# Optimization experiments

Measured on AMD Instinct MI355X. Metric: run time of the kernel, lower is better.

## Reference

```python
import math
import jax, jax.numpy as jnp
import numpy as np

B, H, HKV, L, S, D = 1, 32, 8, 2048, 2048, 128
N_REP = H // HKV          # 4
SCALE = 1.0 / math.sqrt(D)


def setup_inputs() -> dict:
    key = jax.random.key(0)
    k1, k2, k3, k4 = jax.random.split(key, 4)
    query = jax.random.normal(k1, (B, H, L, D), dtype=jnp.float32)
    k_ = jax.random.normal(k2, (B, HKV, S, D), dtype=jnp.float32)
    v_ = jax.random.normal(k3, (B, HKV, S, D), dtype=jnp.float32)
    attn_mask = jax.random.normal(k4, (B, 1, L, S), dtype=jnp.float32)
    return {"query": query, "key": k_, "value": v_, "attn_mask": attn_mask}


def reference(query, key, value, attn_mask):
    # repeat_kv: Q -> [B, HKV, n_rep, L, D]; K/V stay [B, HKV, S, D]
    # (the torch code reshapes K/V to [B, HKV, 1, S, D]; broadcasting via
    # einsum is equivalent), mask unsqueezed at dim 1 -> [B, 1, 1, L, S].
    q = query.reshape(B, HKV, N_REP, L, D)
    scores = jnp.einsum("bkrld,bksd->bkrls", q, key)          # [B,HKV,n_rep,L,S]
    scores = scores + attn_mask[:, None]                        # broadcast add
    # softmax_fp8(x, dim=-1, invAttnHead=1/sqrt(D)) scales input by invAttnHead
    w = jax.nn.softmax(scores * SCALE, axis=-1)
    # dropout_p = 0.0 -> identity
    out = jnp.einsum("bkrls,bksd->bkrld", w, value)             # [B,HKV,n_rep,L,D]
    return out
```

## Files before the change

### kernel.cpp

```cpp
#include <hip/hip_runtime.h>

#define NH   32
#define NKV  8
#define LQ   2048
#define SK   2048
#define DH   128
#define BM   128
#define BN   64
#define KSTRIDE 136
#define VSTRIDE 72
#define PSTRIDE 72

typedef __attribute__((ext_vector_type(8)))  short bf8;
typedef __attribute__((ext_vector_type(4)))  float f4;
typedef __attribute__((ext_vector_type(16))) float f16v;

#if __has_builtin(__builtin_amdgcn_exp2f)
#define EXP2F(x) __builtin_amdgcn_exp2f(x)
#else
#define EXP2F(x) exp2f(x)
#endif

__device__ __forceinline__ unsigned short f2bf(float f) {
    unsigned int u = __builtin_bit_cast(unsigned int, f);
    u = (u + 0x7FFFu + ((u >> 16) & 1u)) >> 16;
    return (unsigned short)u;
}

__global__ __launch_bounds__(256) void convert_k_kernel(
    const float* __restrict__ K, unsigned short* __restrict__ Kb)
{
    size_t base = ((size_t)blockIdx.x * 256 + threadIdx.x) * 8;
    float4 a = *(const float4*)(K + base);
    float4 b = *(const float4*)(K + base + 4);
    bf8 o;
    o[0] = (short)f2bf(a.x); o[1] = (short)f2bf(a.y);
    o[2] = (short)f2bf(a.z); o[3] = (short)f2bf(a.w);
    o[4] = (short)f2bf(b.x); o[5] = (short)f2bf(b.y);
    o[6] = (short)f2bf(b.z); o[7] = (short)f2bf(b.w);
    *(bf8*)(Kb + base) = o;
}

__global__ __launch_bounds__(256) void transpose_v_kernel(
    const float* __restrict__ V, unsigned short* __restrict__ VTb)
{
    __shared__ __align__(16) unsigned short Vl[DH * VSTRIDE];
    const int tid = threadIdx.x;
    const int kv  = blockIdx.x >> 5;
    const int s0  = (blockIdx.x & 31) * 64;
    const float* Vh = V + (size_t)kv * SK * DH;

    #pragma unroll
    for (int i = 0; i < 8; ++i) {
        int idx = tid * 4 + i * 1024;
        int s = idx >> 7, d = idx & 127;
        const float4 v4 = *(const float4*)(Vh + (size_t)(s0 + s) * DH + d);
        Vl[(d + 0) * VSTRIDE + s] = f2bf(v4.x);
        Vl[(d + 1) * VSTRIDE + s] = f2bf(v4.y);
        Vl[(d + 2) * VSTRIDE + s] = f2bf(v4.z);
        Vl[(d + 3) * VSTRIDE + s] = f2bf(v4.w);
    }
    __syncthreads();
    unsigned short* out = VTb + (size_t)kv * DH * SK;
    #pragma unroll
    for (int i = 0; i < 4; ++i) {
        int c = tid + i * 256;
        int d = c >> 3, s8 = (c & 7) * 8;
        *(bf8*)(out + (size_t)d * SK + s0 + s8) = *(const bf8*)(Vl + d * VSTRIDE + s8);
    }
}

__global__ __launch_bounds__(256, 2) void fattn_kernel(
    const float* __restrict__ Q, const unsigned short* __restrict__ Kb,
    const unsigned short* __restrict__ VTb, const float* __restrict__ M,
    float* __restrict__ O)
{
    __shared__ __align__(16) unsigned short Klds[BN * KSTRIDE];
    __shared__ __align__(16) unsigned short Vlds[DH * VSTRIDE];
    __shared__ __align__(16) unsigned short Plds[4 * 32 * PSTRIDE];

    const int tid  = threadIdx.x;
    const int wave = tid >> 6;
    const int lane = tid & 63;
    const int l32  = lane & 31;
    const int hh   = lane >> 5;

    const int bx = blockIdx.x;
    const int h  = bx >> 4;
    const int lt = bx & 15;
    const int q0 = lt * BM;
    const int kv = h >> 2;

    const float*          Qh  = Q   + (size_t)h  * LQ * DH;
    const unsigned short* Kh  = Kb  + (size_t)kv * SK * DH;
    const unsigned short* VTh = VTb + (size_t)kv * DH * SK;

    const int qrow = q0 + wave * 32 + l32;
    const float* Mq = M + (size_t)qrow * SK;

    bf8 bQ[8];
    #pragma unroll
    for (int ks = 0; ks < 8; ++ks) {
        const float* qp = Qh + (size_t)qrow * DH + ks * 16 + hh * 8;
        float4 a = *(const float4*)(qp);
        float4 b = *(const float4*)(qp + 4);
        bQ[ks][0] = (short)f2bf(a.x); bQ[ks][1] = (short)f2bf(a.y);
        bQ[ks][2] = (short)f2bf(a.z); bQ[ks][3] = (short)f2bf(a.w);
        bQ[ks][4] = (short)f2bf(b.x); bQ[ks][5] = (short)f2bf(b.y);
        bQ[ks][6] = (short)f2bf(b.z); bQ[ks][7] = (short)f2bf(b.w);
    }

    f16v accO[4];
    #pragma unroll
    for (int nt = 0; nt < 4; ++nt)
        #pragma unroll
        for (int r = 0; r < 16; ++r) accO[nt][r] = 0.f;
    float lpart = 0.f;

    const float scale_log2e = 0.08838834764831845f * 1.4426950408889634f;

    unsigned short* Pw = Plds + wave * 32 * PSTRIDE;

    for (int s0 = 0; s0 < SK; s0 += BN) {
        __syncthreads();
        #pragma unroll
        for (int c = 0; c < 4; ++c) {
            int chunk = tid + c * 256;
            int sK = chunk >> 4, dK = (chunk & 15) * 8;
            *(bf8*)(Klds + sK * KSTRIDE + dK) =
                *(const bf8*)(Kh + (size_t)(s0 + sK) * DH + dK);
            int dV = chunk >> 3, sV = (chunk & 7) * 8;
            *(bf8*)(Vlds + dV * VSTRIDE + sV) =
                *(const bf8*)(VTh + (size_t)dV * SK + s0 + sV);
        }
        float4 mv[2][4];
        #pragma unroll
        for (int mt = 0; mt < 2; ++mt)
            #pragma unroll
            for (int grp = 0; grp < 4; ++grp)
                mv[mt][grp] = *(const float4*)(Mq + s0 + mt * 32 + grp * 8 + hh * 4);
        __syncthreads();

        f16v accS[2];
        #pragma unroll
        for (int mt = 0; mt < 2; ++mt) {
            f16v a;
            #pragma unroll
            for (int r = 0; r < 16; ++r) a[r] = 0.f;
            #pragma unroll
            for (int ks = 0; ks < 8; ++ks) {
                bf8 aK = *(const bf8*)(Klds + (mt * 32 + l32) * KSTRIDE + ks * 16 + hh * 8);
                a = __builtin_amdgcn_mfma_f32_32x32x16_bf16(aK, bQ[ks], a, 0, 0, 0);
            }
            accS[mt] = a;
        }

        #pragma unroll
        for (int mt = 0; mt < 2; ++mt) {
            #pragma unroll
            for (int grp = 0; grp < 4; ++grp) {
                ushort4 pk;
                float e0 = EXP2F((accS[mt][grp * 4 + 0] + mv[mt][grp].x) * scale_log2e);
                float e1 = EXP2F((accS[mt][grp * 4 + 1] + mv[mt][grp].y) * scale_log2e);
                float e2 = EXP2F((accS[mt][grp * 4 + 2] + mv[mt][grp].z) * scale_log2e);
                float e3 = EXP2F((accS[mt][grp * 4 + 3] + mv[mt][grp].w) * scale_log2e);
                lpart += (e0 + e1) + (e2 + e3);
                pk.x = f2bf(e0); pk.y = f2bf(e1); pk.z = f2bf(e2); pk.w = f2bf(e3);
                *(ushort4*)(Pw + l32 * PSTRIDE + mt * 32 + grp * 8 + hh * 4) = pk;
            }
        }
        asm volatile("s_waitcnt lgkmcnt(0)" ::: "memory");

        bf8 bP[4];
        #pragma unroll
        for (int ks = 0; ks < 4; ++ks)
            bP[ks] = *(const bf8*)(Pw + l32 * PSTRIDE + ks * 16 + hh * 8);
        #pragma unroll
        for (int nt = 0; nt < 4; ++nt) {
            f16v a = accO[nt];
            #pragma unroll
            for (int ks = 0; ks < 4; ++ks) {
                bf8 aV = *(const bf8*)(Vlds + (nt * 32 + l32) * VSTRIDE + ks * 16 + hh * 8);
                a = __builtin_amdgcn_mfma_f32_32x32x16_bf16(aV, bP[ks], a, 0, 0, 0);
            }
            accO[nt] = a;
        }
    }

    float l = lpart + __shfl_xor(lpart, 32);
    float inv = 1.0f / l;
    float* Op = O + (size_t)h * LQ * DH + (size_t)qrow * DH;
    #pragma unroll
    for (int nt = 0; nt < 4; ++nt) {
        #pragma unroll
        for (int grp = 0; grp < 4; ++grp) {
            int d = nt * 32 + grp * 8 + hh * 4;
            float4 o;
            o.x = accO[nt][grp * 4 + 0] * inv;
            o.y = accO[nt][grp * 4 + 1] * inv;
            o.z = accO[nt][grp * 4 + 2] * inv;
            o.w = accO[nt][grp * 4 + 3] * inv;
            *(float4*)(Op + d) = o;
        }
    }
}

extern "C" void kernel_launch(void* const* d_in, const int* in_sizes, int n_in,
                              void* d_out, int out_size, void* d_ws, size_t ws_size,
                              hipStream_t stream) {
    const float* Q = (const float*)d_in[0];
    const float* K = (const float*)d_in[1];
    const float* V = (const float*)d_in[2];
    const float* M = (const float*)d_in[3];
    float* O = (float*)d_out;

    unsigned short* Kb  = (unsigned short*)d_ws;
    unsigned short* VTb = Kb + (size_t)NKV * SK * DH;

    convert_k_kernel<<<dim3((NKV * SK * DH) / (256 * 8)), 256, 0, stream>>>(K, Kb);
    transpose_v_kernel<<<dim3(NKV * (SK / 64)), 256, 0, stream>>>(V, VTb);

    dim3 grid(NH * (LQ / BM));
    fattn_kernel<<<grid, 256, 0, stream>>>(Q, Kb, VTb, M, O);
}
```

Measured before the change: 206.4 us.

## Split KV tile across wave pairs with BM=64 and reduce partial outputs in LDS

Halves the query tile to 64 rows and splits each 64-key tile between two wave pairs. Each wave computes a 32x32 score block and a partial PV product, and the two halves are summed through shared memory at the end. This doubles the grid size and raises the occupancy hint to 3 blocks per CU to improve latency hiding and load balance. In exchange, every loaded K/V tile is reused by half as many query rows, so K/V traffic per block goes up, and an extra LDS reduction is added.

```diff
diff --git a/kernel.cpp b/kernel.cpp
--- a/kernel.cpp
+++ b/kernel.cpp
@@ -5,11 +5,11 @@
 #define LQ   2048
 #define SK   2048
 #define DH   128
-#define BM   128
+#define BM   64
 #define BN   64
 #define KSTRIDE 136
 #define VSTRIDE 72
-#define PSTRIDE 72
+#define PSTRIDE 40
 
 typedef __attribute__((ext_vector_type(8)))  short bf8;
 typedef __attribute__((ext_vector_type(4)))  float f4;
@@ -70,24 +70,29 @@
     }
 }
 
-__global__ __launch_bounds__(256, 2) void fattn_kernel(
+__global__ __launch_bounds__(256, 3) void fattn_kernel(
     const float* __restrict__ Q, const unsigned short* __restrict__ Kb,
     const unsigned short* __restrict__ VTb, const float* __restrict__ M,
     float* __restrict__ O)
 {
-    __shared__ __align__(16) unsigned short Klds[BN * KSTRIDE];
-    __shared__ __align__(16) unsigned short Vlds[DH * VSTRIDE];
-    __shared__ __align__(16) unsigned short Plds[4 * 32 * PSTRIDE];
+    __shared__ __align__(16) unsigned short SMEM[23040];
+    unsigned short* Klds = SMEM;
+    unsigned short* Vlds = SMEM + 8704;
+    unsigned short* Plds = SMEM + 17920;
+    float* R  = (float*)SMEM;
+    float* R2 = (float*)(SMEM + 17920);
 
     const int tid  = threadIdx.x;
     const int wave = tid >> 6;
     const int lane = tid & 63;
     const int l32  = lane & 31;
     const int hh   = lane >> 5;
+    const int qg   = wave & 1;
+    const int sh   = wave >> 1;
 
     const int bx = blockIdx.x;
-    const int h  = bx >> 4;
-    const int lt = bx & 15;
+    const int h  = bx >> 5;
+    const int lt = bx & 31;
     const int q0 = lt * BM;
     const int kv = h >> 2;
 
@@ -95,8 +100,8 @@
     const unsigned short* Kh  = Kb  + (size_t)kv * SK * DH;
     const unsigned short* VTh = VTb + (size_t)kv * DH * SK;
 
-    const int qrow = q0 + wave * 32 + l32;
-    const float* Mq = M + (size_t)qrow * SK;
+    const int qrow = q0 + qg * 32 + l32;
+    const float* Mq = M + (size_t)qrow * SK + sh * 32;
 
     bf8 bQ[8];
     #pragma unroll
@@ -121,86 +126,96 @@
 
     unsigned short* Pw = Plds + wave * 32 * PSTRIDE;
 
-    for (int s0 = 0; s0 < SK; s0 += BN) {
+    for (int s0i = 0; s0i < SK; s0i += BN) {
         __syncthreads();
         #pragma unroll
         for (int c = 0; c < 4; ++c) {
             int chunk = tid + c * 256;
             int sK = chunk >> 4, dK = (chunk & 15) * 8;
             *(bf8*)(Klds + sK * KSTRIDE + dK) =
-                *(const bf8*)(Kh + (size_t)(s0 + sK) * DH + dK);
+                *(const bf8*)(Kh + (size_t)(s0i + sK) * DH + dK);
             int dV = chunk >> 3, sV = (chunk & 7) * 8;
             *(bf8*)(Vlds + dV * VSTRIDE + sV) =
-                *(const bf8*)(VTh + (size_t)dV * SK + s0 + sV);
-        }
-        float4 mv[2][4];
-        #pragma unroll
-        for (int mt = 0; mt < 2; ++mt)
-            #pragma unroll
-            for (int grp = 0; grp < 4; ++grp)
-                mv[mt][grp] = *(const float4*)(Mq + s0 + mt * 32 + grp * 8 + hh * 4);
+                *(const bf8*)(VTh + (size_t)dV * SK + s0i + sV);
+        }
+        float4 mv[4];
+        #pragma unroll
+        for (int g = 0; g < 4; ++g)
+            mv[g] = *(const float4*)(Mq + s0i + g * 8 + hh * 4);
         __syncthreads();
 
-        f16v accS[2];
-        #pragma unroll
-        for (int mt = 0; mt < 2; ++mt) {
-            f16v a;
-            #pragma unroll
-            for (int r = 0; r < 16; ++r) a[r] = 0.f;
-            #pragma unroll
-            for (int ks = 0; ks < 8; ++ks) {
-                bf8 aK = *(const bf8*)(Klds + (mt * 32 + l32) * KSTRIDE + ks * 16 + hh * 8);
-                a = __builtin_amdgcn_mfma_f32_32x32x16_bf16(aK, bQ[ks], a, 0, 0, 0);
-            }
-            accS[mt] = a;
-        }
-
-        #pragma unroll
-        for (int mt = 0; mt < 2; ++mt) {
-            #pragma unroll
-            for (int grp = 0; grp < 4; ++grp) {
-                ushort4 pk;
-                float e0 = EXP2F((accS[mt][grp * 4 + 0] + mv[mt][grp].x) * scale_log2e);
-                float e1 = EXP2F((accS[mt][grp * 4 + 1] + mv[mt][grp].y) * scale_log2e);
-                float e2 = EXP2F((accS[mt][grp * 4 + 2] + mv[mt][grp].z) * scale_log2e);
-                float e3 = EXP2F((accS[mt][grp * 4 + 3] + mv[mt][grp].w) * scale_log2e);
-                lpart += (e0 + e1) + (e2 + e3);
-                pk.x = f2bf(e0); pk.y = f2bf(e1); pk.z = f2bf(e2); pk.w = f2bf(e3);
-                *(ushort4*)(Pw + l32 * PSTRIDE + mt * 32 + grp * 8 + hh * 4) = pk;
-            }
+        f16v accS;
+        #pragma unroll
+        for (int r = 0; r < 16; ++r) accS[r] = 0.f;
+        #pragma unroll
+        for (int ks = 0; ks < 8; ++ks) {
+            bf8 aK = *(const bf8*)(Klds + (sh * 32 + l32) * KSTRIDE + ks * 16 + hh * 8);
+            accS = __builtin_amdgcn_mfma_f32_32x32x16_bf16(aK, bQ[ks], accS, 0, 0, 0);
+        }
+
+        #pragma unroll
+        for (int g = 0; g < 4; ++g) {
+            ushort4 pk;
+            float e0 = EXP2F((accS[g * 4 + 0] + mv[g].x) * scale_log2e);
+            float e1 = EXP2F((accS[g * 4 + 1] + mv[g].y) * scale_log2e);
+            float e2 = EXP2F((accS[g * 4 + 2] + mv[g].z) * scale_log2e);
+            float e3 = EXP2F((accS[g * 4 + 3] + mv[g].w) * scale_log2e);
+            lpart += (e0 + e1) + (e2 + e3);
+            pk.x = f2bf(e0); pk.y = f2bf(e1); pk.z = f2bf(e2); pk.w = f2bf(e3);
+            *(ushort4*)(Pw + l32 * PSTRIDE + g * 8 + hh * 4) = pk;
         }
         asm volatile("s_waitcnt lgkmcnt(0)" ::: "memory");
 
-        bf8 bP[4];
-        #pragma unroll
-        for (int ks = 0; ks < 4; ++ks)
-            bP[ks] = *(const bf8*)(Pw + l32 * PSTRIDE + ks * 16 + hh * 8);
+        bf8 bP[2];
+        #pragma unroll
+        for (int k2 = 0; k2 < 2; ++k2)
+            bP[k2] = *(const bf8*)(Pw + l32 * PSTRIDE + k2 * 16 + hh * 8);
         #pragma unroll
         for (int nt = 0; nt < 4; ++nt) {
             f16v a = accO[nt];
             #pragma unroll
-            for (int ks = 0; ks < 4; ++ks) {
-                bf8 aV = *(const bf8*)(Vlds + (nt * 32 + l32) * VSTRIDE + ks * 16 + hh * 8);
-                a = __builtin_amdgcn_mfma_f32_32x32x16_bf16(aV, bP[ks], a, 0, 0, 0);
+            for (int k2 = 0; k2 < 2; ++k2) {
+                bf8 aV = *(const bf8*)(Vlds + (nt * 32 + l32) * VSTRIDE + sh * 32 + k2 * 16 + hh * 8);
+                a = __builtin_amdgcn_mfma_f32_32x32x16_bf16(aV, bP[k2], a, 0, 0, 0);
             }
             accO[nt] = a;
         }
     }
 
-    float l = lpart + __shfl_xor(lpart, 32);
-    float inv = 1.0f / l;
-    float* Op = O + (size_t)h * LQ * DH + (size_t)qrow * DH;
-    #pragma unroll
-    for (int nt = 0; nt < 4; ++nt) {
-        #pragma unroll
-        for (int grp = 0; grp < 4; ++grp) {
-            int d = nt * 32 + grp * 8 + hh * 4;
-            float4 o;
-            o.x = accO[nt][grp * 4 + 0] * inv;
-            o.y = accO[nt][grp * 4 + 1] * inv;
-            o.z = accO[nt][grp * 4 + 2] * inv;
-            o.w = accO[nt][grp * 4 + 3] * inv;
-            *(float4*)(Op + d) = o;
+    __syncthreads();
+    if (sh == 1) {
+        float* Rw = R + qg * 4096 + lane * 16;
+        #pragma unroll
+        for (int nt = 0; nt < 4; ++nt) {
+            #pragma unroll
+            for (int c = 0; c < 4; ++c) {
+                f4 v = {accO[nt][c * 4 + 0], accO[nt][c * 4 + 1],
+                        accO[nt][c * 4 + 2], accO[nt][c * 4 + 3]};
+                *(f4*)(Rw + nt * 1024 + c * 4) = v;
+            }
+        }
+        R2[qg * 64 + lane] = lpart;
+    }
+    __syncthreads();
+    if (sh == 0) {
+        float lsum = lpart + R2[qg * 64 + lane];
+        lsum += __shfl_xor(lsum, 32);
+        float inv = 1.0f / lsum;
+        const float* Rr = R + qg * 4096 + lane * 16;
+        float* Op = O + (size_t)h * LQ * DH + (size_t)qrow * DH;
+        #pragma unroll
+        for (int nt = 0; nt < 4; ++nt) {
+            #pragma unroll
+            for (int g = 0; g < 4; ++g) {
+                f4 p = *(const f4*)(Rr + nt * 1024 + g * 4);
+                int d = nt * 32 + g * 8 + hh * 4;
+                float4 o;
+                o.x = (accO[nt][g * 4 + 0] + p[0]) * inv;
+                o.y = (accO[nt][g * 4 + 1] + p[1]) * inv;
+                o.z = (accO[nt][g * 4 + 2] + p[2]) * inv;
+                o.w = (accO[nt][g * 4 + 3] + p[3]) * inv;
+                *(float4*)(Op + d) = o;
+            }
         }
     }
 }
```

After: 322.1 us. 1.56x slower.
